# Performance work log

Measured on AMD Instinct MI355X. Metric: run time of the kernel, lower is better.

The kernel has to match this reference:

```python
import jax, jax.numpy as jnp
import numpy as np

D_MODEL = 768
H = 12
D_K = D_MODEL // H
B = 2
S = 2048
NEG = -1e9


def setup_inputs() -> dict:
    key = jax.random.key(0)
    ks = jax.random.split(key, 12)
    scale = 1.0 / np.sqrt(D_MODEL)
    inp = {
        "q": jax.random.normal(ks[0], (B, S, D_MODEL), jnp.float32),
        "k": jax.random.normal(ks[1], (B, S, D_MODEL), jnp.float32),
        "v": jax.random.normal(ks[2], (B, S, D_MODEL), jnp.float32),
        "mask": jax.random.randint(ks[3], (B, 1, S, S), 0, 2, jnp.int32),
        "Wq": jax.random.normal(ks[4], (D_MODEL, D_MODEL), jnp.float32) * scale,
        "bq": jnp.zeros((D_MODEL,), jnp.float32),
        "Wk": jax.random.normal(ks[5], (D_MODEL, D_MODEL), jnp.float32) * scale,
        "bk": jnp.zeros((D_MODEL,), jnp.float32),
        "Wv": jax.random.normal(ks[6], (D_MODEL, D_MODEL), jnp.float32) * scale,
        "bv": jnp.zeros((D_MODEL,), jnp.float32),
        "Wo": jax.random.normal(ks[7], (D_MODEL, D_MODEL), jnp.float32) * scale,
        "bo": jnp.zeros((D_MODEL,), jnp.float32),
    }
    return inp


def _split_heads(x):
    # [B, S, D] -> [B, H, S, D_K]
    b, s, _ = x.shape
    return x.reshape(b, s, H, D_K).transpose(0, 2, 1, 3)


def reference(q, k, v, mask, Wq, bq, Wk, bk, Wv, bv, Wo, bo):
    # torch Linear: x @ W.T + b
    query = _split_heads(q @ Wq.T + bq)
    key_ = _split_heads(k @ Wk.T + bk)
    value = _split_heads(v @ Wv.T + bv)

    scores = jnp.einsum("bhqd,bhkd->bhqk", query, key_) / np.sqrt(D_K)
    scores = jnp.where(mask == 0, NEG, scores)
    attn = jax.nn.softmax(scores, axis=-1)  # dropout p=0.0 -> identity

    x = jnp.einsum("bhqk,bhkd->bhqd", attn, value)
    x = x.transpose(0, 2, 1, 3).reshape(q.shape[0], -1, D_MODEL)
    return x @ Wo.T + bo
```

## Files before the change

kernel.cpp:

```cpp
#include <hip/hip_runtime.h>
#include <math.h>

#define DMODEL 768
#define NHEAD 12
#define DKDIM 64
#define BB 2
#define SS 2048
#define MROWS (BB * SS)
#define WELEM (DMODEL * DMODEL)
#define MWORDS (SS / 64)
#define NIT (SS / 64)

typedef unsigned short bf16_t;
typedef __attribute__((ext_vector_type(8))) short s8;
typedef __attribute__((ext_vector_type(4))) float f4;

#define MFMA(a, b, c) __builtin_amdgcn_mfma_f32_16x16x32_bf16((a), (b), (c), 0, 0, 0)

__device__ __forceinline__ bf16_t f2bf(float f) {
    unsigned u = __float_as_uint(f);
    u += 0x7fffu + ((u >> 16) & 1u);
    return (bf16_t)(u >> 16);
}
__device__ __forceinline__ unsigned cvtpk2(float a, float b) {
    unsigned r;
    asm("v_cvt_pk_bf16_f32 %0, %1, %2" : "=v"(r) : "v"(a), "v"(b));
    return r;
}
__device__ __forceinline__ s8 ldfrag(const bf16_t* p) {
    union { uint4 u; s8 s; } x;
    x.u = *(const uint4*)p;
    return x.s;
}

__device__ __forceinline__ void ld_stage(const bf16_t* p, uint4& u0, uint4& u1) {
    u0 = *(const uint4*)p;
    u1 = *(const uint4*)(p + 8);
}
__device__ __forceinline__ void ld_stage(const float* p, uint4& u0, uint4& u1) {
    const float4 f0 = *(const float4*)p;
    const float4 f1 = *(const float4*)(p + 4);
    const float4 f2 = *(const float4*)(p + 8);
    const float4 f3 = *(const float4*)(p + 12);
    u0.x = cvtpk2(f0.x, f0.y); u0.y = cvtpk2(f0.z, f0.w);
    u0.z = cvtpk2(f1.x, f1.y); u0.w = cvtpk2(f1.z, f1.w);
    u1.x = cvtpk2(f2.x, f2.y); u1.y = cvtpk2(f2.z, f2.w);
    u1.z = cvtpk2(f3.x, f3.y); u1.w = cvtpk2(f3.z, f3.w);
}

__global__ void cvt_weights(const float* __restrict__ W0, const float* __restrict__ W1,
                            const float* __restrict__ W2, const float* __restrict__ W3,
                            bf16_t* __restrict__ dst)
{
    const float* src = (blockIdx.y == 0) ? W0 : (blockIdx.y == 1) ? W1
                     : (blockIdx.y == 2) ? W2 : W3;
    bf16_t* d = dst + (size_t)blockIdx.y * WELEM;
    const int i = (blockIdx.x * 256 + threadIdx.x) * 4;
    const float4 v = *(const float4*)(src + i);
    uint2 h;
    h.x = cvtpk2(v.x, v.y);
    h.y = cvtpk2(v.z, v.w);
    *(uint2*)(d + i) = h;
}

__global__ __launch_bounds__(256) void mask_to_bits(
    const int* __restrict__ mask, unsigned long long* __restrict__ mbits)
{
    const size_t gid = (size_t)blockIdx.x * 256 + threadIdx.x;
    const int m = mask[gid];
    const unsigned long long bal = __ballot(m != 0);
    if ((threadIdx.x & 63) == 0) mbits[gid >> 6] = bal;
}

template<typename TA, typename TO>
__global__ __launch_bounds__(256) void gemm_tiled(
    const TA* __restrict__ A0, const TA* __restrict__ A1, const TA* __restrict__ A2,
    const bf16_t* __restrict__ W0, const bf16_t* __restrict__ W1, const bf16_t* __restrict__ W2,
    const float* __restrict__ bias0, const float* __restrict__ bias1, const float* __restrict__ bias2,
    TO* __restrict__ C0, TO* __restrict__ C1, TO* __restrict__ C2,
    float sc0, float sc1, float sc2)
{
    __shared__ uint4 As4[128 * 4];
    __shared__ uint4 Bs4[128 * 4];

    const int z = blockIdx.z;
    const TA*     A    = (z == 0) ? A0 : (z == 1) ? A1 : A2;
    const bf16_t* W    = (z == 0) ? W0 : (z == 1) ? W1 : W2;
    const float*  bias = (z == 0) ? bias0 : (z == 1) ? bias1 : bias2;
    TO*           C    = (z == 0) ? C0 : (z == 1) ? C1 : C2;
    const float   sc   = (z == 0) ? sc0 : (z == 1) ? sc1 : sc2;

    const int tid  = threadIdx.x;
    const int lane = tid & 63;
    const int w    = tid >> 6;
    const int wm   = w & 1;
    const int wn   = w >> 1;
    const int l15  = lane & 15;
    const int quad = lane >> 4;
    const int m0   = blockIdx.y * 128;
    const int n0   = blockIdx.x * 128;

    const int srow  = tid >> 1;
    const int shalf = tid & 1;
    const int sw    = srow & 3;

    const TA*     aptr = A + (size_t)(m0 + srow) * DMODEL + shalf * 16;
    const bf16_t* wptr = W + (size_t)(n0 + srow) * DMODEL + shalf * 16;

    f4 acc[4][4];
    #pragma unroll
    for (int i = 0; i < 4; i++)
        #pragma unroll
        for (int j = 0; j < 4; j++)
            acc[i][j] = (f4){0.f, 0.f, 0.f, 0.f};

    for (int k0 = 0; k0 < DMODEL; k0 += 32) {
        uint4 au0, au1, bu0, bu1;
        ld_stage(aptr + k0, au0, au1);
        ld_stage(wptr + k0, bu0, bu1);
        __syncthreads();
        As4[srow * 4 + ((shalf * 2 + 0) ^ sw)] = au0;
        As4[srow * 4 + ((shalf * 2 + 1) ^ sw)] = au1;
        Bs4[srow * 4 + ((shalf * 2 + 0) ^ sw)] = bu0;
        Bs4[srow * 4 + ((shalf * 2 + 1) ^ sw)] = bu1;
        __syncthreads();

        s8 af[4], bf[4];
        #pragma unroll
        for (int t = 0; t < 4; t++) {
            const int ar = wm * 64 + t * 16 + l15;
            const int br = wn * 64 + t * 16 + l15;
            union { uint4 u; s8 s; } xa, xb;
            xa.u = As4[ar * 4 + (quad ^ (ar & 3))];
            xb.u = Bs4[br * 4 + (quad ^ (br & 3))];
            af[t] = xa.s;
            bf[t] = xb.s;
        }
        #pragma unroll
        for (int mt = 0; mt < 4; mt++)
            #pragma unroll
            for (int nt = 0; nt < 4; nt++)
                acc[mt][nt] = MFMA(af[mt], bf[nt], acc[mt][nt]);
    }

    #pragma unroll
    for (int mt = 0; mt < 4; mt++) {
        #pragma unroll
        for (int nt = 0; nt < 4; nt++) {
            const int col = n0 + wn * 64 + nt * 16 + l15;
            const float bb = bias[col];
            #pragma unroll
            for (int reg = 0; reg < 4; reg++) {
                const int row = m0 + wm * 64 + mt * 16 + quad * 4 + reg;
                const float val = (acc[mt][nt][reg] + bb) * sc;
                TO* dst = C + (size_t)row * DMODEL + col;
                if constexpr (sizeof(TO) == 2) *dst = f2bf(val);
                else                           *dst = val;
            }
        }
    }
}

__global__ __launch_bounds__(256) void attn_mfma(
    const bf16_t* __restrict__ Q, const bf16_t* __restrict__ K,
    const bf16_t* __restrict__ V, const unsigned long long* __restrict__ mbits,
    bf16_t* __restrict__ O)
{
    __shared__ unsigned Vs[2][64][36];
    __shared__ unsigned Ps[4][16][36];

    const int tid  = threadIdx.x;
    const int lane = tid & 63;
    const int w    = tid >> 6;
    const int l15  = lane & 15;
    const int quad = lane >> 4;
    const int q0   = blockIdx.x * 64;
    const int h    = blockIdx.y;
    const int b    = blockIdx.z;
    const size_t base = ((size_t)b * SS) * DMODEL + (size_t)h * DKDIM;

    const bf16_t* qrow = Q + base + (size_t)(q0 + w * 16 + l15) * DMODEL + quad * 8;
    const s8 qf0 = ldfrag(qrow);
    const s8 qf1 = ldfrag(qrow + 32);

    f4 oacc[4];
    float l_part[4];
    #pragma unroll
    for (int i = 0; i < 4; i++) {
        oacc[i] = (f4){0.f, 0.f, 0.f, 0.f};
        l_part[i] = 0.0f;
    }

    const int kp  = tid & 31;
    const int oct = tid >> 5;
    const bf16_t* vbase = V + base + (size_t)(2 * kp) * DMODEL + oct * 8;
    const bf16_t* kbase = K + base + (size_t)l15 * DMODEL + quad * 8;

    const unsigned long long* mbase =
        mbits + ((size_t)b * SS + (q0 + w * 16 + quad * 4)) * MWORDS;

    uint4 va = *(const uint4*)(vbase);
    uint4 vb = *(const uint4*)(vbase + DMODEL);
    {
        const unsigned short* pa = (const unsigned short*)&va;
        const unsigned short* pb = (const unsigned short*)&vb;
        #pragma unroll
        for (int i = 0; i < 8; i++)
            Vs[0][oct * 8 + i][kp] = (unsigned)pa[i] | ((unsigned)pb[i] << 16);
    }
    va = *(const uint4*)(vbase + (size_t)64 * DMODEL);
    vb = *(const uint4*)(vbase + (size_t)64 * DMODEL + DMODEL);

    s8 kf0[4], kf1[4];
    unsigned long long mw[4];
    #pragma unroll
    for (int nt = 0; nt < 4; nt++) {
        const bf16_t* krow = kbase + (size_t)(nt * 16) * DMODEL;
        kf0[nt] = ldfrag(krow);
        kf1[nt] = ldfrag(krow + 32);
    }
    #pragma unroll
    for (int reg = 0; reg < 4; reg++)
        mw[reg] = mbase[(size_t)reg * MWORDS];

    __syncthreads();

    for (int it = 0; it < NIT; ++it) {
        const int k0  = it * 64;
        const int cur = it & 1;

        if (it + 1 < NIT) {
            const unsigned short* pa = (const unsigned short*)&va;
            const unsigned short* pb = (const unsigned short*)&vb;
            #pragma unroll
            for (int i = 0; i < 8; i++)
                Vs[cur ^ 1][oct * 8 + i][kp] = (unsigned)pa[i] | ((unsigned)pb[i] << 16);
            if (it + 2 < NIT) {
                va = *(const uint4*)(vbase + (size_t)(k0 + 128) * DMODEL);
                vb = *(const uint4*)(vbase + (size_t)(k0 + 128) * DMODEL + DMODEL);
            }
        }

        f4 sacc[4];
        __builtin_amdgcn_s_setprio(1);
        #pragma unroll
        for (int nt = 0; nt < 4; nt++) {
            f4 zz = {0.f, 0.f, 0.f, 0.f};
            zz = MFMA(qf0, kf0[nt], zz);
            zz = MFMA(qf1, kf1[nt], zz);
            sacc[nt] = zz;
        }
        __builtin_amdgcn_s_setprio(0);

        unsigned long long mwc[4];
        #pragma unroll
        for (int reg = 0; reg < 4; reg++) mwc[reg] = mw[reg];
        if (it + 1 < NIT) {
            #pragma unroll
            for (int nt = 0; nt < 4; nt++) {
                const bf16_t* krow = kbase + (size_t)(k0 + 64 + nt * 16) * DMODEL;
                kf0[nt] = ldfrag(krow);
                kf1[nt] = ldfrag(krow + 32);
            }
            #pragma unroll
            for (int reg = 0; reg < 4; reg++)
                mw[reg] = mbase[(size_t)reg * MWORDS + it + 1];
        }

        #pragma unroll
        for (int reg = 0; reg < 4; reg++) {
            const unsigned mlo = ((unsigned)mwc[reg]) >> l15;
            const unsigned mhi = ((unsigned)(mwc[reg] >> 32)) >> l15;
            float p[4];
            p[0] = (mlo & 1u)       ? __expf(sacc[0][reg]) : 0.0f;
            p[1] = (mlo & 0x10000u) ? __expf(sacc[1][reg]) : 0.0f;
            p[2] = (mhi & 1u)       ? __expf(sacc[2][reg]) : 0.0f;
            p[3] = (mhi & 0x10000u) ? __expf(sacc[3][reg]) : 0.0f;
            l_part[reg] += (p[0] + p[1]) + (p[2] + p[3]);

            #pragma unroll
            for (int nt = 0; nt < 4; nt++) {
                const float mine  = p[nt];
                const float other = __shfl_xor(mine, 1, 16);
                if ((lane & 1) == 0)
                    Ps[w][quad * 4 + reg][nt * 8 + (l15 >> 1)] = cvtpk2(mine, other);
            }
        }

        __builtin_amdgcn_s_setprio(1);
        #pragma unroll
        for (int kt = 0; kt < 2; kt++) {
            union { uint4 u; s8 s; } pf;
            pf.u = *(const uint4*)&Ps[w][l15][kt * 16 + quad * 4];
            #pragma unroll
            for (int dt = 0; dt < 4; dt++) {
                union { uint4 u; s8 s; } vf;
                vf.u = *(const uint4*)&Vs[cur][dt * 16 + l15][kt * 16 + quad * 4];
                oacc[dt] = MFMA(pf.s, vf.s, oacc[dt]);
            }
        }
        __builtin_amdgcn_s_setprio(0);

        __syncthreads();
    }

    #pragma unroll
    for (int reg = 0; reg < 4; reg++) {
        float rs = l_part[reg];
        rs += __shfl_xor(rs, 1, 16);
        rs += __shfl_xor(rs, 2, 16);
        rs += __shfl_xor(rs, 4, 16);
        rs += __shfl_xor(rs, 8, 16);
        const float inv = 1.0f / rs;
        const size_t row = q0 + w * 16 + quad * 4 + reg;
        #pragma unroll
        for (int dt = 0; dt < 4; dt++) {
            O[base + row * DMODEL + dt * 16 + l15] = f2bf(oacc[dt][reg] * inv);
        }
    }
}

extern "C" void kernel_launch(void* const* d_in, const int* in_sizes, int n_in,
                              void* d_out, int out_size, void* d_ws, size_t ws_size,
                              hipStream_t stream)
{
    const float* q    = (const float*)d_in[0];
    const float* k    = (const float*)d_in[1];
    const float* v    = (const float*)d_in[2];
    const int*   mask = (const int*)  d_in[3];
    const float* Wq   = (const float*)d_in[4];
    const float* bq   = (const float*)d_in[5];
    const float* Wk   = (const float*)d_in[6];
    const float* bk   = (const float*)d_in[7];
    const float* Wv   = (const float*)d_in[8];
    const float* bv   = (const float*)d_in[9];
    const float* Wo   = (const float*)d_in[10];
    const float* bo   = (const float*)d_in[11];
    float* out = (float*)d_out;

    bf16_t* wsb = (bf16_t*)d_ws;
    const size_t plane = (size_t)MROWS * DMODEL;
    bf16_t* Qp  = wsb;
    bf16_t* Kp  = wsb + plane;
    bf16_t* Vp  = wsb + 2 * plane;
    bf16_t* Ctx = wsb + 3 * plane;
    bf16_t* Wqb = wsb + 4 * plane;
    bf16_t* Wkb = Wqb + WELEM;
    bf16_t* Wvb = Wkb + WELEM;
    bf16_t* Wob = Wvb + WELEM;
    unsigned long long* mbits = (unsigned long long*)(Wob + WELEM);

    cvt_weights<<<dim3(WELEM / 1024, 4), 256, 0, stream>>>(Wq, Wk, Wv, Wo, Wqb);
    mask_to_bits<<<dim3((BB * SS * SS) / 256), 256, 0, stream>>>(mask, mbits);

    gemm_tiled<float, bf16_t><<<dim3(DMODEL / 128, MROWS / 128, 3), 256, 0, stream>>>(
        q, k, v, Wqb, Wkb, Wvb, bq, bk, bv, Qp, Kp, Vp, 0.125f, 1.0f, 1.0f);

    attn_mfma<<<dim3(SS / 64, NHEAD, BB), 256, 0, stream>>>(Qp, Kp, Vp, mbits, Ctx);

    gemm_tiled<bf16_t, float><<<dim3(DMODEL / 128, MROWS / 128, 1), 256, 0, stream>>>(
        Ctx, Ctx, Ctx, Wob, Wob, Wob, bo, bo, bo, out, out, out, 1.0f, 1.0f, 1.0f);
}
```

Before: 340.6 us.

## Pre-convert inputs to bf16 and stage QKV GEMM tiles via direct global-to-LDS loads

Adds a separate kernel that converts q/k/v from fp32 to bf16 ahead of time, so the QKV projection GEMM can use global_load_lds to copy tiles straight into shared memory instead of loading through registers and converting inline. The softmax scale is folded together with log2(e) into the Q projection so attention can call exp2 in place of exp. The extra conversion pass adds a full read and write of the inputs plus one more launch. The new GEMM loop has no double buffering, so each k-step waits on its loads behind two barriers.

Result: faster. 332.6 us (-2.4%).

```diff
diff --git a/kernel.cpp b/kernel.cpp
--- a/kernel.cpp
+++ b/kernel.cpp
@@ -32,20 +32,16 @@
     x.u = *(const uint4*)p;
     return x.s;
 }
+__device__ __forceinline__ void gload16(const bf16_t* g, bf16_t* l) {
+    __builtin_amdgcn_global_load_lds(
+        (__attribute__((address_space(1))) void*)g,
+        (__attribute__((address_space(3))) void*)l,
+        16, 0, 0);
+}
 
 __device__ __forceinline__ void ld_stage(const bf16_t* p, uint4& u0, uint4& u1) {
     u0 = *(const uint4*)p;
     u1 = *(const uint4*)(p + 8);
-}
-__device__ __forceinline__ void ld_stage(const float* p, uint4& u0, uint4& u1) {
-    const float4 f0 = *(const float4*)p;
-    const float4 f1 = *(const float4*)(p + 4);
-    const float4 f2 = *(const float4*)(p + 8);
-    const float4 f3 = *(const float4*)(p + 12);
-    u0.x = cvtpk2(f0.x, f0.y); u0.y = cvtpk2(f0.z, f0.w);
-    u0.z = cvtpk2(f1.x, f1.y); u0.w = cvtpk2(f1.z, f1.w);
-    u1.x = cvtpk2(f2.x, f2.y); u1.y = cvtpk2(f2.z, f2.w);
-    u1.z = cvtpk2(f3.x, f3.y); u1.w = cvtpk2(f3.z, f3.w);
 }
 
 __global__ void cvt_weights(const float* __restrict__ W0, const float* __restrict__ W1,
@@ -57,10 +53,22 @@
     bf16_t* d = dst + (size_t)blockIdx.y * WELEM;
     const int i = (blockIdx.x * 256 + threadIdx.x) * 4;
     const float4 v = *(const float4*)(src + i);
-    uint2 h;
-    h.x = cvtpk2(v.x, v.y);
-    h.y = cvtpk2(v.z, v.w);
-    *(uint2*)(d + i) = h;
+    ushort4 h;
+    h.x = f2bf(v.x); h.y = f2bf(v.y); h.z = f2bf(v.z); h.w = f2bf(v.w);
+    *(ushort4*)(d + i) = h;
+}
+
+__global__ __launch_bounds__(256) void cvt_inputs(
+    const float* __restrict__ A0, const float* __restrict__ A1,
+    const float* __restrict__ A2, bf16_t* __restrict__ dst)
+{
+    const float* src = (blockIdx.y == 0) ? A0 : (blockIdx.y == 1) ? A1 : A2;
+    bf16_t* d = dst + (size_t)blockIdx.y * MROWS * DMODEL;
+    const int i = (blockIdx.x * 256 + threadIdx.x) * 4;
+    const float4 v = *(const float4*)(src + i);
+    ushort4 h;
+    h.x = f2bf(v.x); h.y = f2bf(v.y); h.z = f2bf(v.z); h.w = f2bf(v.w);
+    *(ushort4*)(d + i) = h;
 }
 
 __global__ __launch_bounds__(256) void mask_to_bits(
@@ -72,22 +80,21 @@
     if ((threadIdx.x & 63) == 0) mbits[gid >> 6] = bal;
 }
 
-template<typename TA, typename TO>
-__global__ __launch_bounds__(256) void gemm_tiled(
-    const TA* __restrict__ A0, const TA* __restrict__ A1, const TA* __restrict__ A2,
+__global__ __launch_bounds__(256) void gemm_qkv(
+    const bf16_t* __restrict__ A0, const bf16_t* __restrict__ A1, const bf16_t* __restrict__ A2,
     const bf16_t* __restrict__ W0, const bf16_t* __restrict__ W1, const bf16_t* __restrict__ W2,
     const float* __restrict__ bias0, const float* __restrict__ bias1, const float* __restrict__ bias2,
-    TO* __restrict__ C0, TO* __restrict__ C1, TO* __restrict__ C2,
+    bf16_t* __restrict__ C0, bf16_t* __restrict__ C1, bf16_t* __restrict__ C2,
     float sc0, float sc1, float sc2)
 {
     __shared__ uint4 As4[128 * 4];
     __shared__ uint4 Bs4[128 * 4];
 
     const int z = blockIdx.z;
-    const TA*     A    = (z == 0) ? A0 : (z == 1) ? A1 : A2;
+    const bf16_t* A    = (z == 0) ? A0 : (z == 1) ? A1 : A2;
     const bf16_t* W    = (z == 0) ? W0 : (z == 1) ? W1 : W2;
     const float*  bias = (z == 0) ? bias0 : (z == 1) ? bias1 : bias2;
-    TO*           C    = (z == 0) ? C0 : (z == 1) ? C1 : C2;
+    bf16_t*       C    = (z == 0) ? C0 : (z == 1) ? C1 : C2;
     const float   sc   = (z == 0) ? sc0 : (z == 1) ? sc1 : sc2;
 
     const int tid  = threadIdx.x;
@@ -100,11 +107,87 @@
     const int m0   = blockIdx.y * 128;
     const int n0   = blockIdx.x * 128;
 
+    const int r0 = tid >> 2,         s0 = (tid & 3) ^ (r0 & 3);
+    const int r1 = 64 + (tid >> 2),  s1 = (tid & 3) ^ (r1 & 3);
+    const bf16_t* aS0 = A + (size_t)(m0 + r0) * DMODEL + s0 * 8;
+    const bf16_t* aS1 = A + (size_t)(m0 + r1) * DMODEL + s1 * 8;
+    const bf16_t* wS0 = W + (size_t)(n0 + r0) * DMODEL + s0 * 8;
+    const bf16_t* wS1 = W + (size_t)(n0 + r1) * DMODEL + s1 * 8;
+    bf16_t* aD0 = (bf16_t*)As4 + w * 512;
+    bf16_t* aD1 = (bf16_t*)As4 + 2048 + w * 512;
+    bf16_t* bD0 = (bf16_t*)Bs4 + w * 512;
+    bf16_t* bD1 = (bf16_t*)Bs4 + 2048 + w * 512;
+
+    f4 acc[4][4];
+    #pragma unroll
+    for (int i = 0; i < 4; i++)
+        #pragma unroll
+        for (int j = 0; j < 4; j++)
+            acc[i][j] = (f4){0.f, 0.f, 0.f, 0.f};
+
+    for (int k0 = 0; k0 < DMODEL; k0 += 32) {
+        __syncthreads();
+        gload16(aS0 + k0, aD0);
+        gload16(aS1 + k0, aD1);
+        gload16(wS0 + k0, bD0);
+        gload16(wS1 + k0, bD1);
+        __syncthreads();
+
+        s8 af[4], bf[4];
+        #pragma unroll
+        for (int t = 0; t < 4; t++) {
+            const int ar = wm * 64 + t * 16 + l15;
+            const int br = wn * 64 + t * 16 + l15;
+            union { uint4 u; s8 s; } xa, xb;
+            xa.u = As4[ar * 4 + (quad ^ (ar & 3))];
+            xb.u = Bs4[br * 4 + (quad ^ (br & 3))];
+            af[t] = xa.s;
+            bf[t] = xb.s;
+        }
+        #pragma unroll
+        for (int mt = 0; mt < 4; mt++)
+            #pragma unroll
+            for (int nt = 0; nt < 4; nt++)
+                acc[mt][nt] = MFMA(af[mt], bf[nt], acc[mt][nt]);
+    }
+
+    #pragma unroll
+    for (int mt = 0; mt < 4; mt++) {
+        #pragma unroll
+        for (int nt = 0; nt < 4; nt++) {
+            const int col = n0 + wn * 64 + nt * 16 + l15;
+            const float bb = bias[col];
+            #pragma unroll
+            for (int reg = 0; reg < 4; reg++) {
+                const int row = m0 + wm * 64 + mt * 16 + quad * 4 + reg;
+                C[(size_t)row * DMODEL + col] = f2bf((acc[mt][nt][reg] + bb) * sc);
+            }
+        }
+    }
+}
+
+__global__ __launch_bounds__(256) void gemm_out(
+    const bf16_t* __restrict__ A, const bf16_t* __restrict__ W,
+    const float* __restrict__ bias, float* __restrict__ C)
+{
+    __shared__ uint4 As4[128 * 4];
+    __shared__ uint4 Bs4[128 * 4];
+
+    const int tid  = threadIdx.x;
+    const int lane = tid & 63;
+    const int w    = tid >> 6;
+    const int wm   = w & 1;
+    const int wn   = w >> 1;
+    const int l15  = lane & 15;
+    const int quad = lane >> 4;
+    const int m0   = blockIdx.y * 128;
+    const int n0   = blockIdx.x * 128;
+
     const int srow  = tid >> 1;
     const int shalf = tid & 1;
     const int sw    = srow & 3;
 
-    const TA*     aptr = A + (size_t)(m0 + srow) * DMODEL + shalf * 16;
+    const bf16_t* aptr = A + (size_t)(m0 + srow) * DMODEL + shalf * 16;
     const bf16_t* wptr = W + (size_t)(n0 + srow) * DMODEL + shalf * 16;
 
     f4 acc[4][4];
@@ -152,10 +235,7 @@
             #pragma unroll
             for (int reg = 0; reg < 4; reg++) {
                 const int row = m0 + wm * 64 + mt * 16 + quad * 4 + reg;
-                const float val = (acc[mt][nt][reg] + bb) * sc;
-                TO* dst = C + (size_t)row * DMODEL + col;
-                if constexpr (sizeof(TO) == 2) *dst = f2bf(val);
-                else                           *dst = val;
+                C[(size_t)row * DMODEL + col] = acc[mt][nt][reg] + bb;
             }
         }
     }
@@ -272,10 +352,10 @@
             const unsigned mlo = ((unsigned)mwc[reg]) >> l15;
             const unsigned mhi = ((unsigned)(mwc[reg] >> 32)) >> l15;
             float p[4];
-            p[0] = (mlo & 1u)       ? __expf(sacc[0][reg]) : 0.0f;
-            p[1] = (mlo & 0x10000u) ? __expf(sacc[1][reg]) : 0.0f;
-            p[2] = (mhi & 1u)       ? __expf(sacc[2][reg]) : 0.0f;
-            p[3] = (mhi & 0x10000u) ? __expf(sacc[3][reg]) : 0.0f;
+            p[0] = (mlo & 1u)       ? __builtin_exp2f(sacc[0][reg]) : 0.0f;
+            p[1] = (mlo & 0x10000u) ? __builtin_exp2f(sacc[1][reg]) : 0.0f;
+            p[2] = (mhi & 1u)       ? __builtin_exp2f(sacc[2][reg]) : 0.0f;
+            p[3] = (mhi & 0x10000u) ? __builtin_exp2f(sacc[3][reg]) : 0.0f;
             l_part[reg] += (p[0] + p[1]) + (p[2] + p[3]);
 
             #pragma unroll
@@ -348,16 +428,18 @@
     bf16_t* Wkb = Wqb + WELEM;
     bf16_t* Wvb = Wkb + WELEM;
     bf16_t* Wob = Wvb + WELEM;
-    unsigned long long* mbits = (unsigned long long*)(Wob + WELEM);
+    bf16_t* Abf = Wob + WELEM;
+    unsigned long long* mbits = (unsigned long long*)(Abf + 3 * plane);
 
     cvt_weights<<<dim3(WELEM / 1024, 4), 256, 0, stream>>>(Wq, Wk, Wv, Wo, Wqb);
+    cvt_inputs<<<dim3((int)(plane / 1024), 3), 256, 0, stream>>>(q, k, v, Abf);
     mask_to_bits<<<dim3((BB * SS * SS) / 256), 256, 0, stream>>>(mask, mbits);
 
-    gemm_tiled<float, bf16_t><<<dim3(DMODEL / 128, MROWS / 128, 3), 256, 0, stream>>>(
-        q, k, v, Wqb, Wkb, Wvb, bq, bk, bv, Qp, Kp, Vp, 0.125f, 1.0f, 1.0f);
+    gemm_qkv<<<dim3(DMODEL / 128, MROWS / 128, 3), 256, 0, stream>>>(
+        Abf, Abf + plane, Abf + 2 * plane, Wqb, Wkb, Wvb, bq, bk, bv,
+        Qp, Kp, Vp, 0.125f * 1.44269504f, 1.0f, 1.0f);
 
     attn_mfma<<<dim3(SS / 64, NHEAD, BB), 256, 0, stream>>>(Qp, Kp, Vp, mbits, Ctx);
 
-    gemm_tiled<bf16_t, float><<<dim3(DMODEL / 128, MROWS / 128, 1), 256, 0, stream>>>(
-        Ctx, Ctx, Ctx, Wob, Wob, Wob, bo, bo, bo, out, out, out, 1.0f, 1.0f, 1.0f);
-}
+    gemm_out<<<dim3(DMODEL / 128, MROWS / 128), 256, 0, stream>>>(Ctx, Wob, bo, out);
+}
```
